# Optimization experiments

Measured on AMD Instinct MI355X. Metric: run time of the kernel, lower is better.

The kernel has to match this reference:

```python
import jax, jax.numpy as jnp
import numpy as np

B, N, F, T, H = 16, 400, 64, 12, 4
HD = F // H  # head dim = 16


def _adj_weights(adj, theta):
    # theta: (N,1). diag -> theta_i ; neighbors of row i -> theta_i / deg_i ; else 0
    eye = jnp.eye(N, dtype=adj.dtype)
    ncount = (adj - eye).sum(axis=1, keepdims=True) + 1e-10  # (N,1)
    neigh = (adj > 0) & (eye == 0)
    return jnp.where(eye > 0, theta, jnp.where(neigh, theta / ncount, jnp.zeros((), adj.dtype)))


def _agg_conv(x, wadj, thA, thB, W1, W2, adj):
    # x: (B,N,F,T), wadj: (B,1,N,N)
    A1 = _adj_weights(adj, thA)
    A2 = _adj_weights(adj, thB)
    xt = x.transpose(0, 3, 1, 2)                      # (B,T,N,F)
    f1 = jnp.matmul(wadj * A1, xt)                    # 1-hop agg (B,T,N,F)
    f2 = jnp.matmul(jnp.matmul(wadj, wadj) * A2, xt)  # 2-hop agg
    out = jax.nn.sigmoid(f1 @ W1 + f2 @ W2)
    return out.transpose(0, 2, 3, 1)                  # (B,N,F,T)


def _mha(xl, Wq, bq, Wk, bk, Wv, bv, Wo, bo):
    # xl: (..., L, F); attention over axis -2
    q, k, v = xl @ Wq + bq, xl @ Wk + bk, xl @ Wv + bv
    sp = lambda t: t.reshape(t.shape[:-1] + (H, HD))
    q, k, v = sp(q), sp(k), sp(v)
    s = jnp.einsum('...qhd,...khd->...hqk', q, k) / (HD ** 0.5)
    a = jax.nn.softmax(s, axis=-1)
    o = jnp.einsum('...hqk,...khd->...qhd', a, v)
    o = o.reshape(o.shape[:-2] + (F,))
    return o @ Wo + bo


def _max_agg(x, W, b, src, dst):
    # x: (B,N,F,T) -> linear on F, then per (B,T) graph max-aggregation over edges
    h = jnp.einsum('bnft,fo->btno', x, W) + b         # (B,T,N,F)
    h = h.reshape(B * T, N, F)
    gathered = h[:, src, :]                            # (BT,E,F)
    agg = jax.vmap(lambda g: jax.ops.segment_max(g, dst, num_segments=N))(gathered)
    return agg.reshape(B, T, N, F).transpose(0, 2, 3, 1)


def _gated_conv(x, tw, tb, gw, gb):
    # x: (B,N,F,T) -> conv along T (kernel (1,3), pad (0,1)) per node
    xc = x.transpose(0, 2, 1, 3)                      # (B,F,N,T)
    dn = ('NCHW', 'OIHW', 'NCHW')
    conv = lambda w, bb: jax.lax.conv_general_dilated(
        xc, w, (1, 1), [(0, 0), (1, 1)], dimension_numbers=dn) + bb[None, :, None, None]
    out = conv(tw, tb) * jax.nn.sigmoid(conv(gw, gb))
    return out.transpose(0, 2, 1, 3)


def setup_inputs() -> dict:
    rng = np.random.default_rng(0)
    A = (rng.random((N, N)) < 8.0 / N).astype(np.float32)
    A = np.maximum(A, A.T)
    np.fill_diagonal(A, 1.0)
    src, dst = np.nonzero(A)
    key = jax.random.key(0)
    ks = iter(jax.random.split(key, 48))
    nrm = lambda shape, s=1.0: jax.random.normal(next(ks), shape, dtype=jnp.float32) * s
    def lin(i, o):
        sc = (1.0 / i) ** 0.5
        return nrm((i, o), sc), jnp.zeros((o,), jnp.float32)
    sq_w, sq_b = lin(F, F); sk_w, sk_b = lin(F, F); sv_w, sv_b = lin(F, F); so_w, so_b = lin(F, F)
    tq_w, tq_b = lin(F, F); tk_w, tk_b = lin(F, F); tv_w, tv_b = lin(F, F); to_w, to_b = lin(F, F)
    mp_w, mp_b = lin(F, F)
    return dict(
        x=nrm((B, N, F, T)),
        weighted_adj=jax.random.uniform(next(ks), (B, 1, N, N), dtype=jnp.float32),
        mask_week=jax.random.uniform(next(ks), (B, N, 1, 1), dtype=jnp.float32),
        mask_day=jax.random.uniform(next(ks), (B, N, 1, 1), dtype=jnp.float32),
        theta1=jnp.full((N, 1), 0.5, jnp.float32), theta2=jnp.full((N, 1), 0.5, jnp.float32),
        theta3=jnp.full((N, 1), 0.5, jnp.float32), theta4=jnp.full((N, 1), 0.5, jnp.float32),
        gw1a=nrm((F, F)), gw1b=nrm((F, F)), gw2a=nrm((F, F)), gw2b=nrm((F, F)),
        mp_w=mp_w, mp_b=mp_b,
        tc_w=nrm((F, F, 1, 3), 0.1), tc_b=jnp.zeros((F,), jnp.float32),
        gc_w=nrm((F, F, 1, 3), 0.1), gc_b=jnp.zeros((F,), jnp.float32),
        sq_w=sq_w, sq_b=sq_b, sk_w=sk_w, sk_b=sk_b, sv_w=sv_w, sv_b=sv_b, so_w=so_w, so_b=so_b,
        tq_w=tq_w, tq_b=tq_b, tk_w=tk_w, tk_b=tk_b, tv_w=tv_w, tv_b=tv_b, to_w=to_w, to_b=to_b,
        ln_g=jnp.ones((F,), jnp.float32), ln_b=jnp.zeros((F,), jnp.float32),
        adj=jnp.asarray(A),
        edge_index=jnp.asarray(np.stack([src, dst]).astype(np.int32)),
        mask=1,
    )


def reference(x, weighted_adj, mask_week, mask_day,
              theta1, theta2, theta3, theta4,
              gw1a, gw1b, gw2a, gw2b, mp_w, mp_b,
              tc_w, tc_b, gc_w, gc_b,
              sq_w, sq_b, sk_w, sk_b, sv_w, sv_b, so_w, so_b,
              tq_w, tq_b, tk_w, tk_b, tv_w, tv_b, to_w, to_b,
              ln_g, ln_b, adj, edge_index, mask):
    src, dst = edge_index[0], edge_index[1]
    # spatial attention: (B,T,N,F) attend over N
    sa = _mha(x.transpose(0, 3, 1, 2), sq_w, sq_b, sk_w, sk_b, sv_w, sv_b, so_w, so_b)
    sa = sa.transpose(0, 2, 3, 1)  # (B,N,F,T)
    # temporal attention: (B,N,T,F) attend over T (dropout is identity in eval)
    ta = _mha(x.transpose(0, 1, 3, 2), tq_w, tq_b, tk_w, tk_b, tv_w, tv_b, to_w, to_b)
    ta = ta.transpose(0, 1, 3, 2)  # (B,N,F,T)

    mean1 = _agg_conv(sa, weighted_adj, theta1, theta2, gw1a, gw1b, adj)
    maxp = _max_agg(mean1, mp_w, mp_b, src, dst)
    mean2 = _agg_conv(maxp, weighted_adj, theta3, theta4, gw2a, gw2b, adj)
    last = mean2 * mask_week * mask_day if mask else mean2

    gated = _gated_conv(ta, tc_w, tc_b, gc_w, gc_b)
    output = last + gated

    r = jax.nn.relu(output + x).transpose(0, 3, 1, 2)  # (B,T,N,F)
    mu = r.mean(axis=-1, keepdims=True)
    var = r.var(axis=-1, keepdims=True)
    r = (r - mu) / jnp.sqrt(var + 1e-5) * ln_g + ln_b
    return r.transpose(0, 2, 3, 1)  # (B,N,F,T)
```

## Files before the change

kernel.cpp:

```cpp
#include <hip/hip_runtime.h>
#include <hip/hip_bf16.h>

constexpr int Bc = 16, Nc = 400, Fc = 64, Tc = 12, NHc = 4, HDc = 16;
constexpr int NN = Nc * Nc;

__global__ void k_rowptr(const int* __restrict__ src, int E, int* __restrict__ rowp) {
    for (int e = threadIdx.x; e < E; e += blockDim.x) {
        int s = src[e];
        if (e == 0 || src[e - 1] != s) rowp[s] = e;
    }
    if (threadIdx.x == 0) rowp[Nc] = E;
}

__global__ void k_transpose(const float* __restrict__ in, float* __restrict__ out) {
    __shared__ float tile[32][33];
    int b = blockIdx.z;
    int x0 = blockIdx.x * 32, y0 = blockIdx.y * 32;
    const float* inb = in + (size_t)b * NN;
    float* outb = out + (size_t)b * NN;
    for (int j = threadIdx.y; j < 32; j += 8) {
        int y = y0 + j, x = x0 + threadIdx.x;
        if (y < Nc && x < Nc) tile[j][threadIdx.x] = inb[y * Nc + x];
    }
    __syncthreads();
    for (int j = threadIdx.y; j < 32; j += 8) {
        int y = x0 + j, x = y0 + threadIdx.x;
        if (y < Nc && x < Nc) outb[y * Nc + x] = tile[threadIdx.x][j];
    }
}

__global__ void k_w2ec(const float* __restrict__ wadj, const float* __restrict__ wadjT,
                       const int* __restrict__ src, const int* __restrict__ dst,
                       const int* __restrict__ rowp, int E,
                       float* __restrict__ cf1, float* __restrict__ cf2) {
    int widx = (blockIdx.x * blockDim.x + threadIdx.x) >> 6;
    int lane = threadIdx.x & 63;
    if (widx >= Bc * E) return;
    int b = widx / E, e = widx % E;
    int i = src[e], j = dst[e];
    const float* ra = wadj + (size_t)b * NN + (size_t)i * Nc;
    const float* rb = wadjT + (size_t)b * NN + (size_t)j * Nc;
    float s = 0.f;
    for (int k = lane; k < Nc; k += 64) s += ra[k] * rb[k];
    for (int off = 32; off; off >>= 1) s += __shfl_xor(s, off, 64);
    if (lane == 0) {
        float deg = (float)(rowp[i + 1] - rowp[i] - 1);
        float sc = (j == i) ? 1.f : 1.f / (deg + 1e-10f);
        cf1[widx] = ra[j] * sc;
        cf2[widx] = s * sc;
    }
}

__global__ __launch_bounds__(384) void k_qkv3(const float* __restrict__ x,
    const float* __restrict__ wq, const float* __restrict__ bq,
    const float* __restrict__ wk, const float* __restrict__ bk,
    const float* __restrict__ wv, const float* __restrict__ bv,
    float* __restrict__ sqkv) {
    __shared__ float xs[8 * 768];
    int blk = blockIdx.x;
    int b = blk / 50, nch = blk % 50;
    int n0 = nch * 8;
    const float* xp = x + ((long)b * Nc + n0) * 768;
    for (int i = threadIdx.x; i < 1536; i += 384)
        ((float4*)xs)[i] = ((const float4*)xp)[i];
    __syncthreads();
    int wid = threadIdx.x >> 6, lane = threadIdx.x & 63;
    int sel = wid % 3, half = wid / 3;
    const float* W = sel == 0 ? wq : sel == 1 ? wk : wv;
    const float* Bb = sel == 0 ? bq : sel == 1 ? bk : bv;
    float wr[64];
#pragma unroll
    for (int f = 0; f < 64; ++f) wr[f] = W[f * 64 + lane];
    float bias = Bb[lane];
    for (int nl = half * 4; nl < half * 4 + 4; ++nl) {
        int n = n0 + nl;
        const float* xrow = xs + nl * 768;
        for (int t0 = 0; t0 < 12; t0 += 4) {
            float a[4] = {bias, bias, bias, bias};
#pragma unroll
            for (int f = 0; f < 64; ++f) {
                float w = wr[f];
                const float* xq = xrow + f * 12 + t0;
                a[0] = fmaf(xq[0], w, a[0]);
                a[1] = fmaf(xq[1], w, a[1]);
                a[2] = fmaf(xq[2], w, a[2]);
                a[3] = fmaf(xq[3], w, a[3]);
            }
#pragma unroll
            for (int i = 0; i < 4; ++i)
                sqkv[(((long)b * 12 + t0 + i) * Nc + n) * 192 + sel * 64 + lane] = a[i];
        }
    }
}

__global__ __launch_bounds__(448) void k_sattn2(const float* __restrict__ sqkv,
                                                float* __restrict__ Os) {
    __shared__ float Kh[Nc * HDc];
    __shared__ float Vh[Nc * HDc];
    int bth = blockIdx.x;
    int h = bth & 3;
    int bt = bth >> 2;
    const float* base = sqkv + (long)bt * Nc * 192;
    for (int i = threadIdx.x; i < 1600; i += 448) {
        int n = i >> 2, r = i & 3;
        ((float4*)Kh)[i] = *(const float4*)(base + n * 192 + 64 + h * 16 + r * 4);
        ((float4*)Vh)[i] = *(const float4*)(base + n * 192 + 128 + h * 16 + r * 4);
    }
    __syncthreads();
    int nq = threadIdx.x;
    if (nq >= Nc) return;
    float q[16];
#pragma unroll
    for (int d = 0; d < 16; ++d) q[d] = base[nq * 192 + h * 16 + d];
    float m = -INFINITY, l = 0.f, acc[16];
#pragma unroll
    for (int d = 0; d < 16; ++d) acc[d] = 0.f;
    for (int k0 = 0; k0 < Nc; k0 += 16) {
        float s[16];
        float tm = -INFINITY;
#pragma unroll
        for (int kk = 0; kk < 16; ++kk) {
            const float* kv = Kh + (k0 + kk) * 16;
            float d0 = 0.f;
#pragma unroll
            for (int d = 0; d < 16; ++d) d0 = fmaf(q[d], kv[d], d0);
            s[kk] = d0 * 0.25f;
            tm = fmaxf(tm, s[kk]);
        }
        if (tm > m) {
            float corr = __expf(m - tm);
            l *= corr;
#pragma unroll
            for (int d = 0; d < 16; ++d) acc[d] *= corr;
            m = tm;
        }
#pragma unroll
        for (int kk = 0; kk < 16; ++kk) {
            float p = __expf(s[kk] - m);
            l += p;
            const float* vv = Vh + (k0 + kk) * 16;
#pragma unroll
            for (int d = 0; d < 16; ++d) acc[d] = fmaf(p, vv[d], acc[d]);
        }
    }
    float inv = 1.f / l;
    float* op = Os + ((long)bt * Nc + nq) * 64 + h * 16;
#pragma unroll
    for (int d = 0; d < 16; ++d) op[d] = acc[d] * inv;
}

__global__ __launch_bounds__(256) void k_proj64b(const float* __restrict__ X,
    const float* __restrict__ W, const float* __restrict__ bias,
    float* __restrict__ Y) {
    __shared__ float xs[64 * 64];
    long r0 = (long)blockIdx.x * 64;
    const float* xp = X + r0 * 64;
    for (int i = threadIdx.x; i < 1024; i += 256)
        ((float4*)xs)[i] = ((const float4*)xp)[i];
    int wid = threadIdx.x >> 6, lane = threadIdx.x & 63;
    float wr[64];
#pragma unroll
    for (int f = 0; f < 64; ++f) wr[f] = W[f * 64 + lane];
    float bv = bias[lane];
    __syncthreads();
    for (int g = 0; g < 4; ++g) {
        int r = wid * 16 + g * 4;
        float a[4] = {bv, bv, bv, bv};
#pragma unroll
        for (int f = 0; f < 64; ++f) {
            float w = wr[f];
            a[0] = fmaf(xs[(r + 0) * 64 + f], w, a[0]);
            a[1] = fmaf(xs[(r + 1) * 64 + f], w, a[1]);
            a[2] = fmaf(xs[(r + 2) * 64 + f], w, a[2]);
            a[3] = fmaf(xs[(r + 3) * 64 + f], w, a[3]);
        }
#pragma unroll
        for (int i = 0; i < 4; ++i) Y[(r0 + r + i) * 64 + lane] = a[i];
    }
}

__global__ __launch_bounds__(512) void k_proj2(const float* __restrict__ X,
    const float* __restrict__ W1, const float* __restrict__ W2,
    float* __restrict__ G1, float* __restrict__ G2) {
    __shared__ float xs[64 * 64];
    long r0 = (long)blockIdx.x * 64;
    const float* xp = X + r0 * 64;
    for (int i = threadIdx.x; i < 1024; i += 512)
        ((float4*)xs)[i] = ((const float4*)xp)[i];
    int wid = threadIdx.x >> 6, lane = threadIdx.x & 63;
    const float* W = (wid & 4) ? W2 : W1;
    float* G = (wid & 4) ? G2 : G1;
    int w4 = wid & 3;
    float wr[64];
#pragma unroll
    for (int f = 0; f < 64; ++f) wr[f] = W[f * 64 + lane];
    __syncthreads();
    for (int g = 0; g < 4; ++g) {
        int r = w4 * 16 + g * 4;
        float a[4] = {0.f, 0.f, 0.f, 0.f};
#pragma unroll
        for (int f = 0; f < 64; ++f) {
            float w = wr[f];
            a[0] = fmaf(xs[(r + 0) * 64 + f], w, a[0]);
            a[1] = fmaf(xs[(r + 1) * 64 + f], w, a[1]);
            a[2] = fmaf(xs[(r + 2) * 64 + f], w, a[2]);
            a[3] = fmaf(xs[(r + 3) * 64 + f], w, a[3]);
        }
#pragma unroll
        for (int i = 0; i < 4; ++i) G[(r0 + r + i) * 64 + lane] = a[i];
    }
}

__global__ __launch_bounds__(256) void k_gath(const float* __restrict__ G1,
    const float* __restrict__ G2, const float* __restrict__ cf1,
    const float* __restrict__ cf2, const int* __restrict__ rowp,
    const int* __restrict__ dst, const float* __restrict__ thA,
    const float* __restrict__ thB, int E, float* __restrict__ Y) {
    int blk = blockIdx.x;
    int bt = blk % 192;
    int n0 = (blk / 192) * 4;
    int b = bt / Tc;
    int nl = threadIdx.x >> 6, lane = threadIdx.x & 63;
    int n = n0 + nl;
    const float* g1 = G1 + (long)bt * Nc * 64;
    const float* g2 = G2 + (long)bt * Nc * 64;
    const float* c1p = cf1 + (size_t)b * E;
    const float* c2p = cf2 + (size_t)b * E;
    int e0 = rowp[n], e1 = rowp[n + 1];
    float a1 = 0.f, a2 = 0.f;
    for (int e = e0; e < e1; ++e) {
        int j = dst[e] * 64 + lane;
        a1 = fmaf(c1p[e], g1[j], a1);
        a2 = fmaf(c2p[e], g2[j], a2);
    }
    float acc = thA[n] * a1 + thB[n] * a2;
    Y[((long)bt * Nc + n) * 64 + lane] = 1.f / (1.f + __expf(-acc));
}

__global__ __launch_bounds__(384) void k_tattn3(const float* __restrict__ x,
    const float* __restrict__ wq, const float* __restrict__ bq,
    const float* __restrict__ wk, const float* __restrict__ bk,
    const float* __restrict__ wv, const float* __restrict__ bv,
    const float* __restrict__ wo, const float* __restrict__ bo,
    float* __restrict__ ta) {
    constexpr int QS = 193;
    __shared__ float xs_ol[3072];
    __shared__ float qs[48 * QS];
    float* xs = xs_ol;
    float* ol = xs_ol;
    int blk = blockIdx.x;
    int b = blk / 100, nch = blk % 100;
    int n0 = nch * 4;
    const float* xp = x + ((long)b * Nc + n0) * 768;
    for (int i = threadIdx.x; i < 768; i += 384)
        ((float4*)xs)[i] = ((const float4*)xp)[i];
    __syncthreads();
    int wid = threadIdx.x >> 6, lane = threadIdx.x & 63;
    {
        int sel = wid % 3, half = wid / 3;
        const float* W = sel == 0 ? wq : sel == 1 ? wk : wv;
        const float* Bb = sel == 0 ? bq : sel == 1 ? bk : bv;
        float wr[64];
#pragma unroll
        for (int f = 0; f < 64; ++f) wr[f] = W[f * 64 + lane];
        float bias = Bb[lane];
        for (int nl = half * 2; nl < half * 2 + 2; ++nl) {
            const float* xrow = xs + nl * 768;
            for (int t0 = 0; t0 < 12; t0 += 4) {
                float a[4] = {bias, bias, bias, bias};
#pragma unroll
                for (int f = 0; f < 64; ++f) {
                    float w = wr[f];
                    const float* xq = xrow + f * 12 + t0;
                    a[0] = fmaf(xq[0], w, a[0]);
                    a[1] = fmaf(xq[1], w, a[1]);
                    a[2] = fmaf(xq[2], w, a[2]);
                    a[3] = fmaf(xq[3], w, a[3]);
                }
#pragma unroll
                for (int i = 0; i < 4; ++i)
                    qs[(nl * 12 + t0 + i) * QS + sel * 64 + lane] = a[i];
            }
        }
    }
    __syncthreads();
    {
        int triple = threadIdx.x >> 1, dh = threadIdx.x & 1;
        int nl = triple / 48, r2 = triple % 48;
        int t = r2 >> 2, h = r2 & 3;
        const float* qv = qs + (nl * 12 + t) * QS + h * 16;
        float s[12];
        float mx = -INFINITY;
#pragma unroll
        for (int k = 0; k < 12; ++k) {
            const float* kv = qs + (nl * 12 + k) * QS + 64 + h * 16;
            float a0 = 0.f;
#pragma unroll
            for (int dd = 0; dd < 16; ++dd) a0 = fmaf(qv[dd], kv[dd], a0);
            s[k] = a0 * 0.25f;
            mx = fmaxf(mx, s[k]);
        }
        float l = 0.f;
#pragma unroll
        for (int k = 0; k < 12; ++k) { s[k] = __expf(s[k] - mx); l += s[k]; }
        float inv = 1.f / l;
#pragma unroll
        for (int dd = 0; dd < 8; ++dd) {
            int d = dh * 8 + dd;
            float o = 0.f;
#pragma unroll
            for (int k = 0; k < 12; ++k)
                o = fmaf(s[k], qs[(nl * 12 + k) * QS + 128 + h * 16 + d], o);
            ol[(nl * 12 + t) * 64 + h * 16 + d] = o * inv;
        }
    }
    __syncthreads();
    {
        float wr[64];
#pragma unroll
        for (int f = 0; f < 64; ++f) wr[f] = wo[f * 64 + lane];
        float ob = bo[lane];
        for (int g = 0; g < 2; ++g) {
            int r = wid * 8 + g * 4;
            float a[4] = {ob, ob, ob, ob};
#pragma unroll
            for (int f = 0; f < 64; ++f) {
                float w = wr[f];
                a[0] = fmaf(ol[(r + 0) * 64 + f], w, a[0]);
                a[1] = fmaf(ol[(r + 1) * 64 + f], w, a[1]);
                a[2] = fmaf(ol[(r + 2) * 64 + f], w, a[2]);
                a[3] = fmaf(ol[(r + 3) * 64 + f], w, a[3]);
            }
#pragma unroll
            for (int i = 0; i < 4; ++i) {
                int rr = r + i;
                int nl = rr / 12, t = rr % 12;
                ta[(((long)b * Nc + n0 + nl) * 12 + t) * 64 + lane] = a[i];
            }
        }
    }
}

__global__ __launch_bounds__(256) void k_segmax(const float* __restrict__ h,
    const int* __restrict__ rowp, const int* __restrict__ dst, float* __restrict__ Y) {
    int blk = blockIdx.x;
    int bt = blk % 192;
    int n0 = (blk / 192) * 4;
    int nl = threadIdx.x >> 6, f = threadIdx.x & 63;
    int n = n0 + nl;
    int e0 = rowp[n], e1 = rowp[n + 1];
    float m = -INFINITY;
    const float* hb = h + (long)bt * Nc * 64;
    for (int e = e0; e < e1; ++e) m = fmaxf(m, hb[dst[e] * 64 + f]);
    Y[((long)bt * Nc + n) * 64 + f] = m;
}

__global__ __launch_bounds__(256) void k_gated2(const float* __restrict__ ta,
    const float* __restrict__ tcw, const float* __restrict__ tcb,
    const float* __restrict__ gcw, const float* __restrict__ gcb,
    float* __restrict__ gated) {
    __shared__ float wl[192 * 65];
    __shared__ float tal[4][64 * 13];
    int wave = threadIdx.x >> 6, lane = threadIdx.x & 63;
    int bn = blockIdx.x * 4 + wave;
    for (int idx = threadIdx.x; idx < 64 * 192; idx += 256) {
        int o = idx / 192, r = idx % 192;
        wl[r * 65 + o] = tcw[idx];
    }
    {
        const float* tr = ta + (long)bn * 768;
        for (int i = lane; i < 768; i += 64) {
            int t = i >> 6, f = i & 63;
            tal[wave][f * 13 + t] = tr[i];
        }
    }
    __syncthreads();
    int o = lane;
    float acc_t[12], acc_g[12];
#pragma unroll
    for (int t = 0; t < 12; ++t) acc_t[t] = tcb[o];
    for (int ic = 0; ic < 64; ++ic) {
        float xe[14];
        xe[0] = 0.f; xe[13] = 0.f;
#pragma unroll
        for (int t = 0; t < 12; ++t) xe[t + 1] = tal[wave][ic * 13 + t];
        float w0 = wl[(ic * 3 + 0) * 65 + o];
        float w1 = wl[(ic * 3 + 1) * 65 + o];
        float w2 = wl[(ic * 3 + 2) * 65 + o];
#pragma unroll
        for (int t = 0; t < 12; ++t)
            acc_t[t] += xe[t] * w0 + xe[t + 1] * w1 + xe[t + 2] * w2;
    }
    __syncthreads();
    for (int idx = threadIdx.x; idx < 64 * 192; idx += 256) {
        int o2 = idx / 192, r = idx % 192;
        wl[r * 65 + o2] = gcw[idx];
    }
    __syncthreads();
#pragma unroll
    for (int t = 0; t < 12; ++t) acc_g[t] = gcb[o];
    for (int ic = 0; ic < 64; ++ic) {
        float xe[14];
        xe[0] = 0.f; xe[13] = 0.f;
#pragma unroll
        for (int t = 0; t < 12; ++t) xe[t + 1] = tal[wave][ic * 13 + t];
        float w0 = wl[(ic * 3 + 0) * 65 + o];
        float w1 = wl[(ic * 3 + 1) * 65 + o];
        float w2 = wl[(ic * 3 + 2) * 65 + o];
#pragma unroll
        for (int t = 0; t < 12; ++t)
            acc_g[t] += xe[t] * w0 + xe[t + 1] * w1 + xe[t + 2] * w2;
    }
    int b = bn / Nc, n = bn % Nc;
#pragma unroll
    for (int t = 0; t < 12; ++t) {
        float g = acc_t[t] * (1.f / (1.f + __expf(-acc_g[t])));
        gated[((long)(b * Tc + t) * Nc + n) * 64 + o] = g;
    }
}

__global__ __launch_bounds__(256) void k_final(const float* __restrict__ mean2,
    const float* __restrict__ gated, const float* __restrict__ x,
    const float* __restrict__ mw, const float* __restrict__ md,
    const float* __restrict__ lng, const float* __restrict__ lnb,
    const int* __restrict__ maskp, float* __restrict__ out) {
    __shared__ float xl[64 * 13];
    __shared__ float rl[64 * 13];
    int bn = blockIdx.x;
    int b = bn / Nc, n = bn % Nc;
    const float* xrow = x + (long)bn * 768;
    for (int i = threadIdx.x; i < 768; i += 256)
        xl[(i / 12) * 13 + (i % 12)] = xrow[i];
    __syncthreads();
    float maskf = maskp[0] ? (mw[bn] * md[bn]) : 1.f;
    int wave = threadIdx.x >> 6, f = threadIdx.x & 63;
    for (int t = wave; t < 12; t += 4) {
        long base = ((long)(b * Tc + t) * Nc + n) * 64;
        float v = mean2[base + f] * maskf + gated[base + f];
        float r = v + xl[f * 13 + t];
        r = fmaxf(r, 0.f);
        float s = r;
        for (int off = 32; off; off >>= 1) s += __shfl_xor(s, off, 64);
        float mu = s * (1.f / 64.f);
        float d = r - mu;
        float vs = d * d;
        for (int off = 32; off; off >>= 1) vs += __shfl_xor(vs, off, 64);
        float var = vs * (1.f / 64.f);
        float y = d * rsqrtf(var + 1e-5f) * lng[f] + lnb[f];
        rl[f * 13 + t] = y;
    }
    __syncthreads();
    float* orow = out + (long)bn * 768;
    for (int i = threadIdx.x; i < 768; i += 256)
        orow[i] = rl[(i / 12) * 13 + (i % 12)];
}

extern "C" void kernel_launch(void* const* d_in, const int* in_sizes, int n_in,
                              void* d_out, int out_size, void* d_ws, size_t ws_size,
                              hipStream_t stream) {
    const float* x    = (const float*)d_in[0];
    const float* wadj = (const float*)d_in[1];
    const float* mw   = (const float*)d_in[2];
    const float* md   = (const float*)d_in[3];
    const float* th1  = (const float*)d_in[4];
    const float* th2  = (const float*)d_in[5];
    const float* th3  = (const float*)d_in[6];
    const float* th4  = (const float*)d_in[7];
    const float* gw1a = (const float*)d_in[8];
    const float* gw1b = (const float*)d_in[9];
    const float* gw2a = (const float*)d_in[10];
    const float* gw2b = (const float*)d_in[11];
    const float* mpw  = (const float*)d_in[12];
    const float* mpb  = (const float*)d_in[13];
    const float* tcw  = (const float*)d_in[14];
    const float* tcb  = (const float*)d_in[15];
    const float* gcw  = (const float*)d_in[16];
    const float* gcb  = (const float*)d_in[17];
    const float* sqw  = (const float*)d_in[18]; const float* sqb = (const float*)d_in[19];
    const float* skw  = (const float*)d_in[20]; const float* skb = (const float*)d_in[21];
    const float* svw  = (const float*)d_in[22]; const float* svb = (const float*)d_in[23];
    const float* sow  = (const float*)d_in[24]; const float* sob = (const float*)d_in[25];
    const float* tqw  = (const float*)d_in[26]; const float* tqb = (const float*)d_in[27];
    const float* tkw  = (const float*)d_in[28]; const float* tkb = (const float*)d_in[29];
    const float* tvw  = (const float*)d_in[30]; const float* tvb = (const float*)d_in[31];
    const float* tow  = (const float*)d_in[32]; const float* tob = (const float*)d_in[33];
    const float* lng  = (const float*)d_in[34]; const float* lnb = (const float*)d_in[35];
    const int* eidx   = (const int*)d_in[37];
    const int* maskp  = (const int*)d_in[38];
    int E = in_sizes[37] / 2;
    const int* esrc = eidx;
    const int* edst = eidx + E;

    const long SZ = (long)Bc * Tc * Nc * 64;
    float* ws = (float*)d_ws;
    float* sqkv  = ws;
    float* Os    = ws + 3 * SZ;
    float* sa    = ws + 4 * SZ;
    float* ta    = ws + 5 * SZ;
    float* wadjT = ws + 6 * SZ;
    float* cf1   = wadjT + (long)Bc * NN;
    float* cf2   = cf1 + (long)Bc * E;
    int*   rowp  = (int*)(cf2 + (long)Bc * E);
    float* g1    = ws;
    float* g2    = ws + SZ;
    float* mean1 = ws + 2 * SZ;
    float* hbuf  = ws;
    float* maxp  = ws + SZ;
    float* g1b   = ws;
    float* g2b   = ws + 2 * SZ;
    float* mean2 = Os;
    float* gatedb= ws + SZ;

    hipLaunchKernelGGL(k_rowptr, dim3(1), dim3(256), 0, stream, esrc, E, rowp);
    hipLaunchKernelGGL(k_transpose, dim3(13, 13, Bc), dim3(32, 8), 0, stream, wadj, wadjT);
    int w2blocks = (Bc * E + 3) / 4;
    hipLaunchKernelGGL(k_w2ec, dim3(w2blocks), dim3(256), 0, stream, wadj, wadjT, esrc, edst, rowp, E, cf1, cf2);
    hipLaunchKernelGGL(k_qkv3, dim3(Bc * 50), dim3(384), 0, stream, x, sqw, sqb, skw, skb, svw, svb, sqkv);
    hipLaunchKernelGGL(k_sattn2, dim3(Bc * Tc * NHc), dim3(448), 0, stream, sqkv, Os);
    hipLaunchKernelGGL(k_proj64b, dim3(1200), dim3(256), 0, stream, Os, sow, sob, sa);
    hipLaunchKernelGGL(k_tattn3, dim3(Bc * 100), dim3(384), 0, stream, x, tqw, tqb, tkw, tkb, tvw, tvb, tow, tob, ta);
    hipLaunchKernelGGL(k_proj2, dim3(1200), dim3(512), 0, stream, sa, gw1a, gw1b, g1, g2);
    hipLaunchKernelGGL(k_gath, dim3(19200), dim3(256), 0, stream, g1, g2, cf1, cf2, rowp, edst, th1, th2, E, mean1);
    hipLaunchKernelGGL(k_proj64b, dim3(1200), dim3(256), 0, stream, mean1, mpw, mpb, hbuf);
    hipLaunchKernelGGL(k_segmax, dim3(19200), dim3(256), 0, stream, hbuf, rowp, edst, maxp);
    hipLaunchKernelGGL(k_proj2, dim3(1200), dim3(512), 0, stream, maxp, gw2a, gw2b, g1b, g2b);
    hipLaunchKernelGGL(k_gath, dim3(19200), dim3(256), 0, stream, g1b, g2b, cf1, cf2, rowp, edst, th3, th4, E, mean2);
    hipLaunchKernelGGL(k_gated2, dim3(1600), dim3(256), 0, stream, ta, tcw, tcb, gcw, gcb, gatedb);
    hipLaunchKernelGGL(k_final, dim3(6400), dim3(256), 0, stream, mean2, gatedb, x, mw, md, lng, lnb, maskp, (float*)d_out);
}
```

Baseline: 895.4 us.

## Double-buffer K/V tiles in spatial attention kernel to overlap loads with compute

The spatial attention kernel previously loaded the full 400-key K and V head slices into shared memory before computing. It now streams them in 80-key tiles through a double-buffered shared-memory scheme, prefetching the next tile while the current one is consumed, and folds the 1/sqrt(d) scale into q once. This cuts shared memory per block, which may allow more resident blocks, and overlaps global loads with compute, at the cost of five block-wide barriers.

```diff
diff --git a/kernel.cpp b/kernel.cpp
--- a/kernel.cpp
+++ b/kernel.cpp
@@ -93,60 +93,84 @@
     }
 }
 
-__global__ __launch_bounds__(448) void k_sattn2(const float* __restrict__ sqkv,
+__global__ __launch_bounds__(448) void k_sattn3(const float* __restrict__ sqkv,
                                                 float* __restrict__ Os) {
-    __shared__ float Kh[Nc * HDc];
-    __shared__ float Vh[Nc * HDc];
+    constexpr int KT = 80;
+    __shared__ float Kb[2][KT * 16];
+    __shared__ float Vb[2][KT * 16];
     int bth = blockIdx.x;
     int h = bth & 3;
     int bt = bth >> 2;
     const float* base = sqkv + (long)bt * Nc * 192;
-    for (int i = threadIdx.x; i < 1600; i += 448) {
-        int n = i >> 2, r = i & 3;
-        ((float4*)Kh)[i] = *(const float4*)(base + n * 192 + 64 + h * 16 + r * 4);
-        ((float4*)Vh)[i] = *(const float4*)(base + n * 192 + 128 + h * 16 + r * 4);
-    }
-    __syncthreads();
     int nq = threadIdx.x;
-    if (nq >= Nc) return;
+    for (int i = threadIdx.x; i < KT * 8; i += 448) {
+        int kv = i >= KT * 4;
+        int j = kv ? i - KT * 4 : i;
+        int n = j >> 2, r = j & 3;
+        float4 v = *(const float4*)(base + n * 192 + (kv ? 128 : 64) + h * 16 + r * 4);
+        if (kv) *(float4*)&Vb[0][n * 16 + r * 4] = v;
+        else    *(float4*)&Kb[0][n * 16 + r * 4] = v;
+    }
     float q[16];
-#pragma unroll
-    for (int d = 0; d < 16; ++d) q[d] = base[nq * 192 + h * 16 + d];
+    if (nq < Nc) {
+#pragma unroll
+        for (int d = 0; d < 16; ++d) q[d] = base[nq * 192 + h * 16 + d] * 0.25f;
+    }
     float m = -INFINITY, l = 0.f, acc[16];
 #pragma unroll
     for (int d = 0; d < 16; ++d) acc[d] = 0.f;
-    for (int k0 = 0; k0 < Nc; k0 += 16) {
-        float s[16];
-        float tm = -INFINITY;
-#pragma unroll
-        for (int kk = 0; kk < 16; ++kk) {
-            const float* kv = Kh + (k0 + kk) * 16;
-            float d0 = 0.f;
-#pragma unroll
-            for (int d = 0; d < 16; ++d) d0 = fmaf(q[d], kv[d], d0);
-            s[kk] = d0 * 0.25f;
-            tm = fmaxf(tm, s[kk]);
-        }
-        if (tm > m) {
-            float corr = __expf(m - tm);
-            l *= corr;
-#pragma unroll
-            for (int d = 0; d < 16; ++d) acc[d] *= corr;
-            m = tm;
-        }
-#pragma unroll
-        for (int kk = 0; kk < 16; ++kk) {
-            float p = __expf(s[kk] - m);
-            l += p;
-            const float* vv = Vh + (k0 + kk) * 16;
-#pragma unroll
-            for (int d = 0; d < 16; ++d) acc[d] = fmaf(p, vv[d], acc[d]);
-        }
-    }
-    float inv = 1.f / l;
-    float* op = Os + ((long)bt * Nc + nq) * 64 + h * 16;
-#pragma unroll
-    for (int d = 0; d < 16; ++d) op[d] = acc[d] * inv;
+    __syncthreads();
+    for (int t = 0; t < 5; ++t) {
+        int cur = t & 1;
+        if (t < 4) {
+            const float* nbase = base + (t + 1) * KT * 192;
+            for (int i = threadIdx.x; i < KT * 8; i += 448) {
+                int kv = i >= KT * 4;
+                int j = kv ? i - KT * 4 : i;
+                int n = j >> 2, r = j & 3;
+                float4 v = *(const float4*)(nbase + n * 192 + (kv ? 128 : 64) + h * 16 + r * 4);
+                if (kv) *(float4*)&Vb[cur ^ 1][n * 16 + r * 4] = v;
+                else    *(float4*)&Kb[cur ^ 1][n * 16 + r * 4] = v;
+            }
+        }
+        if (nq < Nc) {
+            for (int c = 0; c < KT; c += 16) {
+                float s[16];
+                float tm = -INFINITY;
+#pragma unroll
+                for (int kk = 0; kk < 16; ++kk) {
+                    const float* kv = &Kb[cur][(c + kk) * 16];
+                    float d0 = 0.f;
+#pragma unroll
+                    for (int d = 0; d < 16; ++d) d0 = fmaf(q[d], kv[d], d0);
+                    s[kk] = d0;
+                    tm = fmaxf(tm, d0);
+                }
+                if (tm > m) {
+                    float corr = __expf(m - tm);
+                    l *= corr;
+#pragma unroll
+                    for (int d = 0; d < 16; ++d) acc[d] *= corr;
+                    m = tm;
+                }
+#pragma unroll
+                for (int kk = 0; kk < 16; ++kk) {
+                    float p = __expf(s[kk] - m);
+                    l += p;
+                    const float* vv = &Vb[cur][(c + kk) * 16];
+#pragma unroll
+                    for (int d = 0; d < 16; ++d) acc[d] = fmaf(p, vv[d], acc[d]);
+                }
+            }
+        }
+        __syncthreads();
+    }
+    if (nq < Nc) {
+        float inv = 1.f / l;
+        float* op = Os + ((long)bt * Nc + nq) * 64 + h * 16;
+#pragma unroll
+        for (int d = 0; d < 16; ++d) op[d] = acc[d] * inv;
+    }
 }
 
 __global__ __launch_bounds__(256) void k_proj64b(const float* __restrict__ X,
@@ -516,7 +540,7 @@
     int w2blocks = (Bc * E + 3) / 4;
     hipLaunchKernelGGL(k_w2ec, dim3(w2blocks), dim3(256), 0, stream, wadj, wadjT, esrc, edst, rowp, E, cf1, cf2);
     hipLaunchKernelGGL(k_qkv3, dim3(Bc * 50), dim3(384), 0, stream, x, sqw, sqb, skw, skb, svw, svb, sqkv);
-    hipLaunchKernelGGL(k_sattn2, dim3(Bc * Tc * NHc), dim3(448), 0, stream, sqkv, Os);
+    hipLaunchKernelGGL(k_sattn3, dim3(Bc * Tc * NHc), dim3(448), 0, stream, sqkv, Os);
     hipLaunchKernelGGL(k_proj64b, dim3(1200), dim3(256), 0, stream, Os, sow, sob, sa);
     hipLaunchKernelGGL(k_tattn3, dim3(Bc * 100), dim3(384), 0, stream, x, tqw, tqb, tkw, tkb, tvw, tvb, tow, tob, ta);
     hipLaunchKernelGGL(k_proj2, dim3(1200), dim3(512), 0, stream, sa, gw1a, gw1b, g1, g2);
```

Result: faster. 871.9 us (-2.6%).
